# Kernel tuning notes

Hardware: AMD Instinct MI355X
Metric: run time of the kernel (lower is better)

## Reference

```python
import jax, jax.numpy as jnp
import numpy as np

D_MODEL = 1024
N_SH = 16            # sub-heads per branch
N_BR = 4             # branches
H_TOT = N_BR * N_SH  # 64 total heads
DH = D_MODEL // N_SH # 64 head dim
BRANCH_CONFIGS = [(16, 0), (128, 16), (128, 0), (512, 144)]


def rms_norm(x):
    eps = jnp.finfo(x.dtype).eps
    return x * jax.lax.rsqrt(jnp.mean(x * x, axis=-1, keepdims=True) + eps)


def rope(x):
    # x: [B, H, T, Dh]; non-standard RoPE: even/odd split, halves concatenated
    T, Dh = x.shape[2], x.shape[3]
    inv_freq = 1.0 / (10000.0 ** (jnp.arange(0, Dh, 2, dtype=jnp.float32) / Dh))
    freqs = jnp.arange(T, dtype=jnp.float32)[:, None] * inv_freq[None, :]  # [T, Dh/2]
    cos = jnp.cos(freqs)[None, None]
    sin = jnp.sin(freqs)[None, None]
    x1 = x[..., 0::2]
    x2 = x[..., 1::2]
    return jnp.concatenate([-x2 * sin + x1 * cos, x1 * sin + x2 * cos], axis=-1)


def setup_inputs() -> dict:
    key = jax.random.key(0)
    ks = jax.random.split(key, 12)
    B, T, C = 2, 1024, D_MODEL
    s = 0.02
    return {
        "X": jax.random.normal(ks[0], (B, T, C), jnp.float32),
        "WQ": jax.random.normal(ks[1], (C, H_TOT * DH), jnp.float32) * s,
        "bQ": jax.random.normal(ks[2], (H_TOT * DH,), jnp.float32) * s,
        "WK": jax.random.normal(ks[3], (C, C), jnp.float32) * s,
        "bK": jax.random.normal(ks[4], (C,), jnp.float32) * s,
        "WV": jax.random.normal(ks[5], (C, H_TOT * DH), jnp.float32) * s,
        "bV": jax.random.normal(ks[6], (H_TOT * DH,), jnp.float32) * s,
        "WO": jax.random.normal(ks[7], (C, C), jnp.float32) * s,
        "bO": jax.random.normal(ks[8], (C,), jnp.float32) * s,
        "sink_scalars": jax.random.normal(ks[9], (H_TOT,), jnp.float32) * s,
        "v_nulls": jax.random.normal(ks[10], (H_TOT, DH), jnp.float32) * s,
    }


def reference(X, WQ, bQ, WK, bK, WV, bV, WO, bO, sink_scalars, v_nulls):
    B, T, C = X.shape
    # projections -> [B, H, T, Dh]
    q = (X @ WQ + bQ).reshape(B, T, H_TOT, DH).transpose(0, 2, 1, 3)
    q = rope(rms_norm(q))
    v = (X @ WV + bV).reshape(B, T, H_TOT, DH).transpose(0, 2, 1, 3)
    k = rope((X @ WK + bK).reshape(B, T, N_SH, DH).transpose(0, 2, 1, 3))
    k = jnp.tile(k, (1, N_BR, 1, 1))  # [B, H_TOT, T, Dh]

    # KMax scores with key self-norm denominator
    scores = jnp.einsum('bhqd,bhkd->bhqk', q, k)
    denom = jnp.sqrt(jnp.sum(k * k, axis=-1))[:, :, None, :]  # [B,H,1,T]
    w = scores / denom

    # banded masks per branch; note: off-band logits become 0 (NOT -inf) -> exp(0)=1 in softmax
    idx = jnp.arange(T)
    dist = idx[:, None] - idx[None, :]  # query - key
    bmasks = jnp.stack([((dist >= g) & (dist < h)).astype(w.dtype)
                        for (h, g) in BRANCH_CONFIGS], axis=0)  # [N_BR,T,T]
    full_mask = jnp.repeat(bmasks, N_SH, axis=0)[None]  # [1,H_TOT,T,T] (band subset of tril)
    w = w * full_mask

    # learnable tanh sink logit per head, concatenated as extra column
    sinks = jnp.broadcast_to(jnp.tanh(sink_scalars).reshape(1, H_TOT, 1, 1), (B, H_TOT, T, 1))
    probs = jax.nn.softmax(jnp.concatenate([w, sinks], axis=-1), axis=-1)

    out = jnp.einsum('bhqk,bhkd->bhqd', probs[..., :T], v)
    out = out + probs[..., T:] * v_nulls.reshape(1, H_TOT, 1, DH)

    # [B,H_TOT,T,Dh] -> [B,N_BR,T,C]
    ctx = out.reshape(B, N_BR, N_SH, T, DH).transpose(0, 1, 3, 2, 4).reshape(B, N_BR, T, C)
    y = ctx @ WO + bO
    return y.mean(axis=1)
```

## Files before the change

### kernel.cpp

```cpp
#include <hip/hip_runtime.h>
#include <hip/hip_bf16.h>
#include <math.h>

#define T_SEQ 1024
#define LOG2_10000 13.287712379549449f

typedef unsigned short u16;
typedef unsigned int u32;
typedef __attribute__((ext_vector_type(8))) short bf16x8;
typedef __attribute__((ext_vector_type(4))) float f32x4;

__device__ __forceinline__ void gload16(const u16* g, const u16* s) {
  __builtin_amdgcn_global_load_lds(
      (const __attribute__((address_space(1))) void*)g,
      (__attribute__((address_space(3))) void*)s, 16, 0, 0);
}

__device__ __forceinline__ u16 f2bf(float x) {
  __hip_bfloat16 h = __float2bfloat16(x);
  return *reinterpret_cast<u16*>(&h);
}
__device__ __forceinline__ float bf2f(u16 x) {
  __hip_bfloat16 h = *reinterpret_cast<__hip_bfloat16*>(&x);
  return __bfloat162float(h);
}

__device__ __forceinline__ void transpose_step(
    const float* __restrict__ W, u16* __restrict__ Wt, int N, int nbx,
    int local, int t, float (*tile)[33]) {
  int bx = local % nbx, by = local / nbx;
  int n0 = bx * 32, k0 = by * 32;
  int r = t >> 3, c4 = (t & 7) * 4;
  float4 v = *reinterpret_cast<const float4*>(&W[(size_t)(k0 + r) * N + n0 + c4]);
  tile[r][c4 + 0] = v.x;
  tile[r][c4 + 1] = v.y;
  tile[r][c4 + 2] = v.z;
  tile[r][c4 + 3] = v.w;
  __syncthreads();
  u16 o[4];
#pragma unroll
  for (int i = 0; i < 4; ++i) o[i] = f2bf(tile[c4 + i][r]);
  *reinterpret_cast<uint2*>(&Wt[(size_t)(n0 + r) * 1024 + k0 + c4]) =
      *reinterpret_cast<const uint2*>(o);
}

__global__ __launch_bounds__(256) void prep_kernel(
    const float* __restrict__ X, const float* __restrict__ WQ,
    const float* __restrict__ WK, const float* __restrict__ WV,
    const float* __restrict__ WO, const float* __restrict__ bQ,
    const float* __restrict__ bV, const float* __restrict__ bK,
    u16* __restrict__ Xb, u16* __restrict__ WQVKt, u16* __restrict__ WOt,
    float* __restrict__ bQVK, float* __restrict__ ctab, float* __restrict__ stab)
{
  __shared__ float tile[32][33];
  const int blk = blockIdx.x, t = threadIdx.x;
  if (blk < 128) {
    int id = blk * 256 + t;
    int tt = id >> 5, p = id & 31;
    float invf = exp2f(-LOG2_10000 * (float)(2 * p) * (1.0f / 64.0f));
    float ang = (float)tt * invf;
    float sn, cs;
    sincosf(ang, &sn, &cs);
    ctab[id] = cs;
    stab[id] = sn;
  } else if (blk < 1152) {
    int i = (blk - 128) * 256 + t;
    float4 a = reinterpret_cast<const float4*>(X)[2 * i];
    float4 b = reinterpret_cast<const float4*>(X)[2 * i + 1];
    u16 o[8] = {f2bf(a.x), f2bf(a.y), f2bf(a.z), f2bf(a.w),
                f2bf(b.x), f2bf(b.y), f2bf(b.z), f2bf(b.w)};
    reinterpret_cast<uint4*>(Xb)[i] = *reinterpret_cast<const uint4*>(o);
  } else if (blk < 5248) {
    transpose_step(WQ, WQVKt, 4096, 128, blk - 1152, t, tile);
  } else if (blk < 9344) {
    transpose_step(WV, WQVKt + (size_t)4096 * 1024, 4096, 128, blk - 5248, t, tile);
  } else if (blk < 10368) {
    transpose_step(WK, WQVKt + (size_t)8192 * 1024, 1024, 32, blk - 9344, t, tile);
  } else if (blk < 11392) {
    transpose_step(WO, WOt, 1024, 32, blk - 10368, t, tile);
  } else {
    int id = (blk - 11392) * 256 + t;
    if (id < 9216)
      bQVK[id] = (id < 4096) ? bQ[id] : (id < 8192) ? bV[id - 4096] : bK[id - 8192];
  }
}

__global__ __launch_bounds__(512, 1) void gemm_qv_kernel(
    const u16* __restrict__ Ab, const u16* __restrict__ Bt,
    const float* __restrict__ bias, u16* __restrict__ Cqv)
{
  __shared__ __align__(16) u16 sA[4][256 * 32];
  __shared__ __align__(16) u16 sB[4][256 * 32];

  const int tid = threadIdx.x;
  const int lane = tid & 63;
  const int w = tid >> 6;
  const int wm = w >> 2, wn = w & 3;
  const int l15 = lane & 15, l4 = lane >> 4;

  const int orig = blockIdx.x;
  const int xcd = orig & 7, j = orig >> 3;
  const int by = (xcd >> 2) * 4 + (j >> 3);
  const int bx = (xcd & 3) * 8 + (j & 7);
  const int m0 = by * 256, n0 = bx * 256;

  const int r0s = tid >> 2,         c0s = tid & 3;
  const int r1s = (512 + tid) >> 2, c1s = (512 + tid) & 3;
  const int sc0 = c0s ^ ((r0s >> 1) & 3);
  const int sc1 = c1s ^ ((r1s >> 1) & 3);
  const u16* aA0 = Ab + (size_t)(m0 + r0s) * 1024 + 8 * sc0;
  const u16* aA1 = Ab + (size_t)(m0 + r1s) * 1024 + 8 * sc1;
  const u16* aB0 = Bt + (size_t)(n0 + r0s) * 1024 + 8 * sc0;
  const u16* aB1 = Bt + (size_t)(n0 + r1s) * 1024 + 8 * sc1;

  const int cp = l4 ^ ((l15 >> 1) & 3);

  f32x4 acc[8][4];
#pragma unroll
  for (int i = 0; i < 8; ++i)
#pragma unroll
    for (int jn = 0; jn < 4; ++jn) acc[i][jn] = (f32x4){0.f, 0.f, 0.f, 0.f};

#define STAGE32(t)                                                             \
  {                                                                            \
    const int sl = (t) & 3;                                                    \
    const int ko = (t) * 32;                                                   \
    gload16(aA0 + ko, &sA[sl][tid * 8]);                                       \
    gload16(aA1 + ko, &sA[sl][4096 + tid * 8]);                                \
    gload16(aB0 + ko, &sB[sl][tid * 8]);                                       \
    gload16(aB1 + ko, &sB[sl][4096 + tid * 8]);                                \
  }

  STAGE32(0);
  STAGE32(1);
#pragma unroll 1
  for (int t = 0; t < 32; ++t) {
    if (t + 2 < 32) {
      STAGE32(t + 2);
      asm volatile("s_waitcnt vmcnt(8)" ::: "memory");
    } else if (t + 1 < 32) {
      asm volatile("s_waitcnt vmcnt(4)" ::: "memory");
    } else {
      asm volatile("s_waitcnt vmcnt(0)" ::: "memory");
    }
    __builtin_amdgcn_sched_barrier(0);
    __builtin_amdgcn_s_barrier();
    __builtin_amdgcn_sched_barrier(0);

    const u16* tA = sA[t & 3];
    const u16* tB = sB[t & 3];

    bf16x8 bf[4];
#pragma unroll
    for (int n = 0; n < 4; ++n) {
      int row = wn * 64 + n * 16 + l15;
      bf[n] = *reinterpret_cast<const bf16x8*>(&tB[row * 32 + cp * 8]);
    }
    bf16x8 af[8];
#pragma unroll
    for (int m = 0; m < 8; ++m) {
      int row = wm * 128 + m * 16 + l15;
      af[m] = *reinterpret_cast<const bf16x8*>(&tA[row * 32 + cp * 8]);
    }
    __builtin_amdgcn_s_setprio(1);
#pragma unroll
    for (int m = 0; m < 8; ++m)
#pragma unroll
      for (int n = 0; n < 4; ++n)
        acc[m][n] = __builtin_amdgcn_mfma_f32_16x16x32_bf16(
            af[m], bf[n], acc[m][n], 0, 0, 0);
    __builtin_amdgcn_s_setprio(0);
  }
#undef STAGE32

#pragma unroll
  for (int n = 0; n < 4; ++n) {
    int col = n0 + wn * 64 + n * 16 + l15;
    float bv = bias[col];
#pragma unroll
    for (int mf = 0; mf < 8; ++mf) {
#pragma unroll
      for (int r = 0; r < 4; ++r) {
        int row = m0 + wm * 128 + mf * 16 + l4 * 4 + r;
        Cqv[(size_t)row * 8192 + col] = f2bf(acc[mf][n][r] + bv);
      }
    }
  }
}

template <bool BF16OUT>
__global__ __launch_bounds__(256) void gemm64_kernel(
    const u16* __restrict__ Ab, const u16* __restrict__ Bt,
    const float* __restrict__ bias, void* __restrict__ Cv,
    int M, int N, int K)
{
  __shared__ __align__(16) u16 sA[2][64 * 64];
  __shared__ __align__(16) u16 sB[2][64 * 64];
  const int tid = threadIdx.x;
  const int lane = tid & 63;
  const int wv = tid >> 6;
  const int wm = wv >> 1, wn = wv & 1;
  const int l15 = lane & 15, l4 = lane >> 4;
  const int m0 = blockIdx.y * 64, n0 = blockIdx.x * 64;

  f32x4 acc[2][2];
#pragma unroll
  for (int i = 0; i < 2; ++i)
#pragma unroll
    for (int j = 0; j < 2; ++j) acc[i][j] = (f32x4){0.f, 0.f, 0.f, 0.f};

  const int r0s = tid >> 3,         c0s = tid & 7;
  const int r1s = (256 + tid) >> 3, c1s = (256 + tid) & 7;
  const int sc0 = c0s ^ (r0s & 7);
  const int sc1 = c1s ^ (r1s & 7);
  const u16* aA0 = Ab + (size_t)(m0 + r0s) * K + 8 * sc0;
  const u16* aA1 = Ab + (size_t)(m0 + r1s) * K + 8 * sc1;
  const u16* aB0 = Bt + (size_t)(n0 + r0s) * K + 8 * sc0;
  const u16* aB1 = Bt + (size_t)(n0 + r1s) * K + 8 * sc1;

  gload16(aA0, &sA[0][tid * 8]);
  gload16(aA1, &sA[0][2048 + tid * 8]);
  gload16(aB0, &sB[0][tid * 8]);
  gload16(aB1, &sB[0][2048 + tid * 8]);

  const int niter = K >> 6;
#pragma unroll 1
  for (int it = 0; it < niter; ++it) {
    const int buf = it & 1;
    __builtin_amdgcn_s_barrier();
    if (it + 1 < niter) {
      const int ko = (it + 1) * 64;
      gload16(aA0 + ko, &sA[buf ^ 1][tid * 8]);
      gload16(aA1 + ko, &sA[buf ^ 1][2048 + tid * 8]);
      gload16(aB0 + ko, &sB[buf ^ 1][tid * 8]);
      gload16(aB1 + ko, &sB[buf ^ 1][2048 + tid * 8]);
      asm volatile("s_waitcnt vmcnt(4)" ::: "memory");
    } else {
      asm volatile("s_waitcnt vmcnt(0)" ::: "memory");
    }
    __builtin_amdgcn_sched_barrier(0);
    bf16x8 af[2][2], bfv[2][2];
#pragma unroll
    for (int kk = 0; kk < 2; ++kk) {
#pragma unroll
      for (int mi = 0; mi < 2; ++mi) {
        int row = wm * 32 + mi * 16 + l15;
        int cs = (kk * 4 + l4) ^ (row & 7);
        af[mi][kk] = *reinterpret_cast<const bf16x8*>(&sA[buf][row * 64 + cs * 8]);
      }
#pragma unroll
      for (int ni = 0; ni < 2; ++ni) {
        int row = wn * 32 + ni * 16 + l15;
        int cs = (kk * 4 + l4) ^ (row & 7);
        bfv[ni][kk] = *reinterpret_cast<const bf16x8*>(&sB[buf][row * 64 + cs * 8]);
      }
    }
#pragma unroll
    for (int kk = 0; kk < 2; ++kk)
#pragma unroll
      for (int mi = 0; mi < 2; ++mi)
#pragma unroll
        for (int ni = 0; ni < 2; ++ni)
          acc[mi][ni] = __builtin_amdgcn_mfma_f32_16x16x32_bf16(
              af[mi][kk], bfv[ni][kk], acc[mi][ni], 0, 0, 0);
  }

#pragma unroll
  for (int mi = 0; mi < 2; ++mi)
#pragma unroll
    for (int ni = 0; ni < 2; ++ni) {
      int col = n0 + wn * 32 + ni * 16 + l15;
      float bv = bias[col];
#pragma unroll
      for (int r = 0; r < 4; ++r) {
        int row = m0 + wm * 32 + mi * 16 + l4 * 4 + r;
        float val = acc[mi][ni][r] + bv;
        size_t idx = (size_t)row * N + col;
        if (BF16OUT) ((u16*)Cv)[idx] = f2bf(val);
        else ((float*)Cv)[idx] = val;
      }
    }
}

__global__ __launch_bounds__(256) void qkvt_kernel(
    u16* __restrict__ QVbf, u16* __restrict__ Kbf,
    const float* __restrict__ ctab, const float* __restrict__ stab,
    float* __restrict__ part)
{
  const int blk = blockIdx.x;
  if (blk < 20480) {
    const int rid  = blk * 8 + (threadIdx.x >> 5);
    const int lane = threadIdx.x & 63;
    const int p    = lane & 31;
    const int gb   = lane & 32;

    u16* row;
    int t;
    const bool isQ = rid < 131072;
    if (isQ) {
      int h = rid & 63, bt = rid >> 6;
      t = bt & 1023;
      row = QVbf + (size_t)bt * 8192 + h * 64;
    } else {
      int r2 = rid - 131072;
      int hsL = r2 & 15, bt = r2 >> 4;
      t = bt & 1023;
      row = Kbf + (size_t)bt * 1024 + hsL * 64;
    }

    u32 v = reinterpret_cast<const u32*>(row)[p];
    float x1 = bf2f((u16)v), x2 = bf2f((u16)(v >> 16));
    float cs = ctab[t * 32 + p], sn = stab[t * 32 + p];

    float o_lo, o_hi;
    if (isQ) {
      float ss = x1 * x1 + x2 * x2;
      ss += __shfl_xor(ss, 1, 64);
      ss += __shfl_xor(ss, 2, 64);
      ss += __shfl_xor(ss, 4, 64);
      ss += __shfl_xor(ss, 8, 64);
      ss += __shfl_xor(ss, 16, 64);
      float rs = rsqrtf(ss * (1.0f / 64.0f) + 1.1920929e-7f);
      float xn1 = x1 * rs, xn2 = x2 * rs;
      o_lo = xn1 * cs - xn2 * sn;
      o_hi = xn1 * sn + xn2 * cs;
    } else {
      float xr1 = x1 * cs - x2 * sn;
      float xr2 = x1 * sn + x2 * cs;
      float ss = xr1 * xr1 + xr2 * xr2;
      ss += __shfl_xor(ss, 1, 64);
      ss += __shfl_xor(ss, 2, 64);
      ss += __shfl_xor(ss, 4, 64);
      ss += __shfl_xor(ss, 8, 64);
      ss += __shfl_xor(ss, 16, 64);
      float rs = rsqrtf(ss);
      o_lo = xr1 * rs;
      o_hi = xr2 * rs;
    }

    int m = (2 * p) & 31;
    float slo0 = __shfl(o_lo, gb + m, 64);
    float slo1 = __shfl(o_lo, gb + m + 1, 64);
    float shi0 = __shfl(o_hi, gb + m, 64);
    float shi1 = __shfl(o_hi, gb + m + 1, 64);
    float e0 = (p < 16) ? slo0 : shi0;
    float e1 = (p < 16) ? slo1 : shi1;
    reinterpret_cast<u32*>(row)[p] = (u32)f2bf(e0) | ((u32)f2bf(e1) << 16);
  } else {
    int vb = blk - 20480;
    int b = vb >> 6, ch = vb & 63;
    const u16* base = QVbf + (size_t)(b * 1024 + ch * 16) * 8192 + 4096;
#pragma unroll
    for (int g = 0; g < 2; ++g) {
      int c0 = (threadIdx.x + g * 256) * 8;
      float s[8] = {0.f, 0.f, 0.f, 0.f, 0.f, 0.f, 0.f, 0.f};
#pragma unroll 4
      for (int r = 0; r < 16; ++r) {
        bf16x8 v = *reinterpret_cast<const bf16x8*>(&base[(size_t)r * 8192 + c0]);
#pragma unroll
        for (int e = 0; e < 8; ++e) s[e] += bf2f((u16)v[e]);
      }
      float* dst = &part[(size_t)vb * 4096 + c0];
#pragma unroll
      for (int e = 0; e < 8; ++e) dst[e] = s[e];
    }
  }
}

__global__ __launch_bounds__(256) void vsum_reduce_kernel(
    const float* __restrict__ part, float* __restrict__ Vsum) {
  int id = blockIdx.x * 256 + threadIdx.x;
  int b = id >> 12, n = id & 4095;
  float s = 0.f;
#pragma unroll 8
  for (int ch = 0; ch < 64; ++ch) s += part[(size_t)(b * 64 + ch) * 4096 + n];
  Vsum[id] = s;
}

__global__ __launch_bounds__(256) void attn_mfma_kernel(
    const u16* __restrict__ Qv, const u16* __restrict__ Kb,
    const float* __restrict__ Vsum, const float* __restrict__ sink,
    const float* __restrict__ vnull, u16* __restrict__ mctxb)
{
  __shared__ __align__(16) u16 sQ[64 * 64];
  __shared__ __align__(16) u16 sK[2][64 * 64];
  __shared__ __align__(16) u16 sVt[2][64 * 64];
  __shared__ __align__(16) u16 sP[64 * 64];

  int blk = blockIdx.x;
  blk = (blk & 7) * 64 + (blk >> 3);
  const int qt  = blk & 15;
  const int hs  = (blk >> 4) & 15;
  const int b   = blk >> 8;
  const int qt0 = qt * 64;

  const int tid  = threadIdx.x;
  const int lane = tid & 63;
  const int wv   = tid >> 6;
  const int l15  = lane & 15;
  const int l4   = lane >> 4;
  const int qr0  = tid >> 3, qi0 = tid & 7;
  const int qr1  = qr0 + 32;
  const int vjp  = tid & 31, vdg = tid >> 5;
  const int qrow = wv * 16 + l15;

  constexpr int HCFG[4] = {16, 128, 128, 512};
  constexpr int GCFG[4] = {0, 16, 0, 144};

  f32x4 macc[4];
#pragma unroll
  for (int i = 0; i < 4; ++i) macc[i] = (f32x4){0.f, 0.f, 0.f, 0.f};

#pragma unroll 1
  for (int br = 0; br < 4; ++br) {
    const int h = br * 16 + hs;
    const int hmax = HCFG[br], g = GCFG[br];
    int klo = qt0 - (hmax - 1); if (klo < 0) klo = 0;
    int khi = qt0 + 63 - g;     if (khi > 1023) khi = 1023;
    const int nc = (khi >= klo) ? ((khi - klo) / 64 + 1) : 0;

    gload16(Qv + (size_t)(b * 1024 + qt0 + qr0) * 8192 + h * 64 + 8 * (qi0 ^ (qr0 & 7)),
            sQ + (size_t)wv * 512);
    gload16(Qv + (size_t)(b * 1024 + qt0 + qr1) * 8192 + h * 64 + 8 * (qi0 ^ (qr1 & 7)),
            sQ + 2048 + (size_t)wv * 512);
    bf16x8 va, vb;
    if (nc > 0) {
      int ja0 = klo + qr0; if (ja0 > 1023) ja0 = 1023;
      int ja1 = klo + qr1; if (ja1 > 1023) ja1 = 1023;
      gload16(Kb + (size_t)(b * 1024 + ja0) * 1024 + hs * 64 + 8 * (qi0 ^ (qr0 & 7)),
              sK[0] + (size_t)wv * 512);
      gload16(Kb + (size_t)(b * 1024 + ja1) * 1024 + hs * 64 + 8 * (qi0 ^ (qr1 & 7)),
              sK[0] + 2048 + (size_t)wv * 512);
      int jva = klo + 2 * vjp, jvb = jva + 1;
      if (jva > 1023) jva = 1023;
      if (jvb > 1023) jvb = 1023;
      va = *reinterpret_cast<const bf16x8*>(
          &Qv[(size_t)(b * 1024 + jva) * 8192 + 4096 + h * 64 + vdg * 8]);
      vb = *reinterpret_cast<const bf16x8*>(
          &Qv[(size_t)(b * 1024 + jvb) * 8192 + 4096 + h * 64 + vdg * 8]);
    }
    asm volatile("s_waitcnt vmcnt(0)" ::: "memory");
    __builtin_amdgcn_sched_barrier(0);
    if (nc > 0) {
#pragma unroll
      for (int e = 0; e < 8; ++e) {
        int d = vdg * 8 + e;
        u32 pack = (u32)(u16)va[e] | ((u32)(u16)vb[e] << 16);
        *reinterpret_cast<u32*>(
            (char*)sVt[0] + d * 128 + ((4 * vjp) ^ ((d & 7) << 4))) = pack;
      }
    }
    asm volatile("s_waitcnt lgkmcnt(0)" ::: "memory");
    __builtin_amdgcn_sched_barrier(0);
    __builtin_amdgcn_s_barrier();

    bf16x8 afQ[2];
#pragma unroll
    for (int kh = 0; kh < 2; ++kh) {
      int cs = (4 * kh + l4) ^ (l15 & 7);
      afQ[kh] = *reinterpret_cast<const bf16x8*>(&sQ[qrow * 64 + cs * 8]);
    }

    f32x4 outv[4];
#pragma unroll
    for (int i = 0; i < 4; ++i) outv[i] = (f32x4){0.f, 0.f, 0.f, 0.f};
    float zacc[4] = {0.f, 0.f, 0.f, 0.f};

    int buf = 0;
#pragma unroll 1
    for (int c = 0; c < nc; ++c) {
      const int j0 = klo + c * 64;
      const bool nxt = (c + 1 < nc);
      if (nxt) {
        int j0n = j0 + 64;
        int ja0 = j0n + qr0; if (ja0 > 1023) ja0 = 1023;
        int ja1 = j0n + qr1; if (ja1 > 1023) ja1 = 1023;
        gload16(Kb + (size_t)(b * 1024 + ja0) * 1024 + hs * 64 + 8 * (qi0 ^ (qr0 & 7)),
                sK[buf ^ 1] + (size_t)wv * 512);
        gload16(Kb + (size_t)(b * 1024 + ja1) * 1024 + hs * 64 + 8 * (qi0 ^ (qr1 & 7)),
                sK[buf ^ 1] + 2048 + (size_t)wv * 512);
        int jva = j0n + 2 * vjp, jvb = jva + 1;
        if (jva > 1023) jva = 1023;
        if (jvb > 1023) jvb = 1023;
        va = *reinterpret_cast<const bf16x8*>(
            &Qv[(size_t)(b * 1024 + jva) * 8192 + 4096 + h * 64 + vdg * 8]);
        vb = *reinterpret_cast<const bf16x8*>(
            &Qv[(size_t)(b * 1024 + jvb) * 8192 + 4096 + h * 64 + vdg * 8]);
      }
      f32x4 sfr[4];
#pragma unroll
      for (int jt = 0; jt < 4; ++jt) {
        int krow = jt * 16 + l15;
        f32x4 acc = (f32x4){0.f, 0.f, 0.f, 0.f};
#pragma unroll
        for (int kh = 0; kh < 2; ++kh) {
          int cs = (4 * kh + l4) ^ (l15 & 7);
          bf16x8 bk = *reinterpret_cast<const bf16x8*>(&sK[buf][krow * 64 + cs * 8]);
          acc = __builtin_amdgcn_mfma_f32_16x16x32_bf16(afQ[kh], bk, acc, 0, 0, 0);
        }
        sfr[jt] = acc;
      }
#pragma unroll
      for (int jt = 0; jt < 4; ++jt) {
        int jloc = jt * 16 + l15;
        int jabs = j0 + jloc;
#pragma unroll
        for (int r = 0; r < 4; ++r) {
          int q_r = wv * 16 + l4 * 4 + r;
          int dist = (qt0 + q_r) - jabs;
          bool inband = (dist >= g) & (dist < hmax) & (jabs < 1024);
          float pv = inband ? (__expf(sfr[jt][r]) - 1.0f) : 0.0f;
          zacc[r] += pv;
          *reinterpret_cast<u16*>(
              (char*)sP + q_r * 128 + ((2 * jloc) ^ ((q_r & 7) << 4))) = f2bf(pv);
        }
      }
      asm volatile("s_waitcnt lgkmcnt(0)" ::: "memory");
      __builtin_amdgcn_sched_barrier(0);
      bf16x8 afP[2];
#pragma unroll
      for (int kh = 0; kh < 2; ++kh) {
        int cs = (4 * kh + l4) ^ (l15 & 7);
        afP[kh] = *reinterpret_cast<const bf16x8*>(&sP[qrow * 64 + cs * 8]);
      }
#pragma unroll
      for (int dt = 0; dt < 4; ++dt) {
        int drow = dt * 16 + l15;
#pragma unroll
        for (int kh = 0; kh < 2; ++kh) {
          int cs = (4 * kh + l4) ^ (l15 & 7);
          bf16x8 bv = *reinterpret_cast<const bf16x8*>(&sVt[buf][drow * 64 + cs * 8]);
          outv[dt] = __builtin_amdgcn_mfma_f32_16x16x32_bf16(afP[kh], bv, outv[dt], 0, 0, 0);
        }
      }
      if (nxt) {
#pragma unroll
        for (int e = 0; e < 8; ++e) {
          int d = vdg * 8 + e;
          u32 pack = (u32)(u16)va[e] | ((u32)(u16)vb[e] << 16);
          *reinterpret_cast<u32*>(
              (char*)sVt[buf ^ 1] + d * 128 + ((4 * vjp) ^ ((d & 7) << 4))) = pack;
        }
      }
      asm volatile("s_waitcnt vmcnt(0) lgkmcnt(0)" ::: "memory");
      __builtin_amdgcn_sched_barrier(0);
      __builtin_amdgcn_s_barrier();
      buf ^= 1;
    }

#pragma unroll
    for (int r = 0; r < 4; ++r) {
      zacc[r] += __shfl_xor(zacc[r], 1, 64);
      zacc[r] += __shfl_xor(zacc[r], 2, 64);
      zacc[r] += __shfl_xor(zacc[r], 4, 64);
      zacc[r] += __shfl_xor(zacc[r], 8, 64);
    }
    float es = __expf(tanhf(sink[h]));
#pragma unroll
    for (int dt = 0; dt < 4; ++dt) {
      int d = dt * 16 + l15;
      float vs = Vsum[(size_t)b * 4096 + h * 64 + d];
      float vn = vnull[h * 64 + d];
#pragma unroll
      for (int r = 0; r < 4; ++r) {
        float invZ = 1.0f / (1024.0f + zacc[r] + es);
        macc[dt][r] += (outv[dt][r] + vs + es * vn) * invZ;
      }
    }
  }

#pragma unroll
  for (int dt = 0; dt < 4; ++dt) {
#pragma unroll
    for (int r = 0; r < 4; ++r) {
      int q_r = wv * 16 + l4 * 4 + r;
      mctxb[(size_t)(b * 1024 + qt0 + q_r) * 1024 + hs * 64 + dt * 16 + l15] =
          f2bf(0.25f * macc[dt][r]);
    }
  }
}

extern "C" void kernel_launch(void* const* d_in, const int* in_sizes, int n_in,
                              void* d_out, int out_size, void* d_ws, size_t ws_size,
                              hipStream_t stream) {
  (void)in_sizes; (void)n_in; (void)out_size; (void)ws_size;
  const float* X    = (const float*)d_in[0];
  const float* WQ   = (const float*)d_in[1];
  const float* bQ   = (const float*)d_in[2];
  const float* WK   = (const float*)d_in[3];
  const float* bK   = (const float*)d_in[4];
  const float* WV   = (const float*)d_in[5];
  const float* bV   = (const float*)d_in[6];
  const float* WO   = (const float*)d_in[7];
  const float* bO   = (const float*)d_in[8];
  const float* sink = (const float*)d_in[9];
  const float* vnul = (const float*)d_in[10];
  float* Y = (float*)d_out;

  char* p = (char*)d_ws;
  u16*   Xb    = (u16*)p;   p += (size_t)2048 * 1024 * 2;
  u16*   WQVKt = (u16*)p;   p += (size_t)9216 * 1024 * 2;
  u16*   WOt   = (u16*)p;   p += (size_t)1024 * 1024 * 2;
  u16*   QVbf  = (u16*)p;   p += (size_t)2048 * 8192 * 2;
  u16*   Kbf   = (u16*)p;   p += (size_t)2048 * 1024 * 2;
  u16*   mctxb = (u16*)p;   p += (size_t)2048 * 1024 * 2;
  float* Vsum  = (float*)p; p += (size_t)2 * 4096 * 4;
  float* vpart = (float*)p; p += (size_t)128 * 4096 * 4;
  float* bQVK  = (float*)p; p += (size_t)9216 * 4;
  float* ctab  = (float*)p; p += (size_t)32768 * 4;
  float* stab  = (float*)p; p += (size_t)32768 * 4;

  dim3 blk(256);
  prep_kernel<<<11428, blk, 0, stream>>>(X, WQ, WK, WV, WO, bQ, bV, bK,
                                         Xb, WQVKt, WOt, bQVK, ctab, stab);

  gemm_qv_kernel<<<256, dim3(512), 0, stream>>>(Xb, WQVKt, bQVK, QVbf);
  gemm64_kernel<true><<<dim3(16, 32), blk, 0, stream>>>(
      Xb, WQVKt + (size_t)8192 * 1024, bQVK + 8192, Kbf, 2048, 1024, 1024);

  qkvt_kernel<<<20608, blk, 0, stream>>>(QVbf, Kbf, ctab, stab, vpart);
  vsum_reduce_kernel<<<32, blk, 0, stream>>>(vpart, Vsum);

  attn_mfma_kernel<<<512, blk, 0, stream>>>(QVbf, Kbf, Vsum, sink, vnul, mctxb);

  gemm64_kernel<false><<<dim3(16, 32), blk, 0, stream>>>(mctxb, WOt, bO, Y, 2048, 1024, 1024);
}
```

Before: 132.7 us.

## Load QV GEMM B operand directly from global into registers, bypassing LDS

The QV projection GEMM no longer stages the B (weight) tile through shared memory. Each wave loads its B fragments straight from global memory into registers, double-buffered one k-step ahead, while A keeps its LDS pipeline. The goal is to halve LDS traffic and footprint and drop the LDS reads of B. The cost is uncoalesced, duplicated global reads of B across the two wm waves and more vector registers, with a changed waitcnt schedule.

```diff
diff --git a/kernel.cpp b/kernel.cpp
--- a/kernel.cpp
+++ b/kernel.cpp
@@ -90,7 +90,6 @@
     const float* __restrict__ bias, u16* __restrict__ Cqv)
 {
   __shared__ __align__(16) u16 sA[4][256 * 32];
-  __shared__ __align__(16) u16 sB[4][256 * 32];
 
   const int tid = threadIdx.x;
   const int lane = tid & 63;
@@ -110,8 +109,11 @@
   const int sc1 = c1s ^ ((r1s >> 1) & 3);
   const u16* aA0 = Ab + (size_t)(m0 + r0s) * 1024 + 8 * sc0;
   const u16* aA1 = Ab + (size_t)(m0 + r1s) * 1024 + 8 * sc1;
-  const u16* aB0 = Bt + (size_t)(n0 + r0s) * 1024 + 8 * sc0;
-  const u16* aB1 = Bt + (size_t)(n0 + r1s) * 1024 + 8 * sc1;
+
+  const u16* bRow[4];
+#pragma unroll
+  for (int n = 0; n < 4; ++n)
+    bRow[n] = Bt + (size_t)(n0 + wn * 64 + n * 16 + l15) * 1024 + l4 * 8;
 
   const int cp = l4 ^ ((l15 >> 1) & 3);
 
@@ -121,57 +123,65 @@
 #pragma unroll
     for (int jn = 0; jn < 4; ++jn) acc[i][jn] = (f32x4){0.f, 0.f, 0.f, 0.f};
 
-#define STAGE32(t)                                                             \
+#define STAGE_A(t)                                                             \
   {                                                                            \
     const int sl = (t) & 3;                                                    \
     const int ko = (t) * 32;                                                   \
     gload16(aA0 + ko, &sA[sl][tid * 8]);                                       \
     gload16(aA1 + ko, &sA[sl][4096 + tid * 8]);                                \
-    gload16(aB0 + ko, &sB[sl][tid * 8]);                                       \
-    gload16(aB1 + ko, &sB[sl][4096 + tid * 8]);                                \
-  }
-
-  STAGE32(0);
-  STAGE32(1);
+  }
+#define BLOAD(dst, t)                                                          \
+  {                                                                            \
+    const int ko = (t) * 32;                                                   \
+    _Pragma("unroll") for (int n = 0; n < 4; ++n)                              \
+        dst[n] = *reinterpret_cast<const bf16x8*>(bRow[n] + ko);               \
+  }
+
+  bf16x8 bE[4], bO[4];
+
+  STAGE_A(0);
+  STAGE_A(1);
+  BLOAD(bE, 0);
+  asm volatile("s_waitcnt vmcnt(0)" ::: "memory");
+  __builtin_amdgcn_sched_barrier(0);
+  __builtin_amdgcn_s_barrier();
+
+#define BODY(t, bcur, bnxt)                                                    \
+  {                                                                            \
+    if ((t) + 1 < 32) BLOAD(bnxt, (t) + 1);                                    \
+    if ((t) + 2 < 32) STAGE_A((t) + 2);                                        \
+    const u16* tA = sA[(t) & 3];                                               \
+    bf16x8 af[8];                                                              \
+    _Pragma("unroll") for (int m = 0; m < 8; ++m) {                            \
+      int row = wm * 128 + m * 16 + l15;                                       \
+      af[m] = *reinterpret_cast<const bf16x8*>(&tA[row * 32 + cp * 8]);        \
+    }                                                                          \
+    __builtin_amdgcn_s_setprio(1);                                             \
+    _Pragma("unroll") for (int m = 0; m < 8; ++m)                              \
+      _Pragma("unroll") for (int n = 0; n < 4; ++n)                            \
+        acc[m][n] = __builtin_amdgcn_mfma_f32_16x16x32_bf16(                   \
+            af[m], bcur[n], acc[m][n], 0, 0, 0);                               \
+    __builtin_amdgcn_s_setprio(0);                                             \
+    if ((t) + 2 < 32) {                                                        \
+      asm volatile("s_waitcnt vmcnt(6)" ::: "memory");                         \
+    } else if ((t) + 1 < 32) {                                                 \
+      asm volatile("s_waitcnt vmcnt(4)" ::: "memory");                         \
+    } else {                                                                   \
+      asm volatile("s_waitcnt vmcnt(0)" ::: "memory");                         \
+    }                                                                          \
+    __builtin_amdgcn_sched_barrier(0);                                         \
+    __builtin_amdgcn_s_barrier();                                              \
+    __builtin_amdgcn_sched_barrier(0);                                         \
+  }
+
 #pragma unroll 1
-  for (int t = 0; t < 32; ++t) {
-    if (t + 2 < 32) {
-      STAGE32(t + 2);
-      asm volatile("s_waitcnt vmcnt(8)" ::: "memory");
-    } else if (t + 1 < 32) {
-      asm volatile("s_waitcnt vmcnt(4)" ::: "memory");
-    } else {
-      asm volatile("s_waitcnt vmcnt(0)" ::: "memory");
-    }
-    __builtin_amdgcn_sched_barrier(0);
-    __builtin_amdgcn_s_barrier();
-    __builtin_amdgcn_sched_barrier(0);
-
-    const u16* tA = sA[t & 3];
-    const u16* tB = sB[t & 3];
-
-    bf16x8 bf[4];
-#pragma unroll
-    for (int n = 0; n < 4; ++n) {
-      int row = wn * 64 + n * 16 + l15;
-      bf[n] = *reinterpret_cast<const bf16x8*>(&tB[row * 32 + cp * 8]);
-    }
-    bf16x8 af[8];
-#pragma unroll
-    for (int m = 0; m < 8; ++m) {
-      int row = wm * 128 + m * 16 + l15;
-      af[m] = *reinterpret_cast<const bf16x8*>(&tA[row * 32 + cp * 8]);
-    }
-    __builtin_amdgcn_s_setprio(1);
-#pragma unroll
-    for (int m = 0; m < 8; ++m)
-#pragma unroll
-      for (int n = 0; n < 4; ++n)
-        acc[m][n] = __builtin_amdgcn_mfma_f32_16x16x32_bf16(
-            af[m], bf[n], acc[m][n], 0, 0, 0);
-    __builtin_amdgcn_s_setprio(0);
-  }
-#undef STAGE32
+  for (int tt = 0; tt < 32; tt += 2) {
+    BODY(tt, bE, bO);
+    BODY(tt + 1, bO, bE);
+  }
+#undef BODY
+#undef BLOAD
+#undef STAGE_A
 
 #pragma unroll
   for (int n = 0; n < 4; ++n) {
```

Result: slower. 149.2 us (+12.5%).
